# Performance work log

Measured on AMD Instinct MI355X. Metric: run time of the kernel, lower is better.

Reference implementation:

```python
import jax, jax.numpy as jnp
import numpy as np

NEG = -1.0e9  # matches torch's masked_fill value
EPS = 1e-12


def setup_inputs() -> dict:
    key = jax.random.key(0)
    ks = jax.random.split(key, 8)
    B, T, S, E, H, M = 128, 512, 512, 256, 1024, 4

    def lin_w(k, fan_in, fan_out):
        lim = 1.0 / np.sqrt(fan_in)
        return jax.random.uniform(k, (fan_in, fan_out), jnp.float32, -lim, lim)

    return {
        "state": jax.random.normal(ks[0], (B, S), jnp.float32),
        "task_features": jax.random.normal(ks[1], (B, T, 5), jnp.float32),
        "nest_ids": jax.random.randint(ks[2], (B, T), 0, M),
        "task_mask": jnp.ones((B, T), jnp.bool_),
        "emb_w": lin_w(ks[3], 5, E),
        "emb_b": jnp.zeros((E,), jnp.float32),
        "w1": lin_w(ks[4], S + E, H),
        "b1": jnp.zeros((H,), jnp.float32),
        "w2": lin_w(ks[5], H, H),
        "b2": jnp.zeros((H,), jnp.float32),
        "w3": lin_w(ks[6], H, 1),
        "b3": jnp.zeros((1,), jnp.float32),
        "etas": jnp.ones((M,), jnp.float32),  # eta_buf (learn_eta=False, eta_init=1.0)
    }


def reference(state, task_features, nest_ids, task_mask,
              emb_w, emb_b, w1, b1, w2, b2, w3, b3, etas):
    B, T, _ = task_features.shape
    M = etas.shape[0]

    # per-task utilities: MLP over concat(state, task_embed)  [B,T]
    te = task_features @ emb_w + emb_b                                # [B,T,E]
    x = jnp.concatenate(
        [jnp.broadcast_to(state[:, None, :], (B, T, state.shape[-1])), te], axis=-1)
    h = jax.nn.relu(x @ w1 + b1)
    h = jax.nn.relu(h @ w2 + b2)
    utils = (h @ w3 + b3)[..., 0]                                     # [B,T]
    utils = jnp.where(task_mask, utils, NEG)

    # nest membership masks (vectorized segment-softmax over nests)
    mem = (nest_ids[..., None] == jnp.arange(M)) & task_mask[..., None]  # [B,T,M]
    nonempty = mem.any(axis=1)                                           # [B,M]

    mval = jnp.max(jnp.where(mem, utils[..., None], -jnp.inf), axis=1)   # [B,M]
    mval = jnp.where(nonempty, mval, 0.0)
    scaled = (utils[..., None] - mval[:, None, :]) / etas                # [B,T,M]
    sums = jnp.sum(jnp.where(mem, jnp.exp(scaled), 0.0), axis=1)         # [B,M]

    # inclusive values U_m = mval + eta_m * log(sum exp((v-mval)/eta_m))
    U = jnp.where(nonempty, mval + etas * jnp.log(jnp.clip(sums, EPS)), NEG)
    p_nest = jax.nn.softmax(U, axis=-1)                                  # [B,M]

    # per-task within-nest probabilities, gathered via nest id
    nid = jnp.clip(nest_ids, 0, M - 1)
    m_t = jnp.take_along_axis(mval, nid, axis=1)                         # [B,T]
    s_t = jnp.take_along_axis(jnp.clip(sums, EPS), nid, axis=1)          # [B,T]
    pn_t = jnp.take_along_axis(p_nest, nid, axis=1)                      # [B,T]
    e_t = jnp.exp((utils - m_t) / etas[nid])
    valid = task_mask & (nest_ids >= 0) & (nest_ids < M)
    p_task = jnp.where(valid, pn_t * e_t / s_t, 0.0)                     # [B,T]

    # degenerate fallback: uniform over valid tasks when everything underflowed
    any_valid = task_mask.any(axis=1)
    fallback = any_valid & (p_task.sum(axis=1) <= EPS)
    uni = 1.0 / jnp.maximum(task_mask.sum(axis=1), 1).astype(p_task.dtype)
    p_task = jnp.where(fallback[:, None] & task_mask, uni[:, None], p_task)

    return utils, p_task, p_nest
```

## Files before the change

kernel.cpp:

```cpp
#include <hip/hip_runtime.h>
#include <stdint.h>

#define NEGV -1.0e9f
#define EPSV 1e-12f

typedef __attribute__((ext_vector_type(8))) short bf16x8;
typedef __attribute__((ext_vector_type(4))) float f32x4;

__device__ __forceinline__ unsigned int f2bf(float f) {
  unsigned int u = __builtin_bit_cast(unsigned int, f);
  u = u + 0x7FFFu + ((u >> 16) & 1u);
  return u >> 16;
}

__device__ __forceinline__ unsigned int cvt_pk_bf16(float lo, float hi) {
  unsigned int r;
  asm("v_cvt_pk_bf16_f32 %0, %1, %2" : "=v"(r) : "v"(lo), "v"(hi));
  return r;
}

__global__ __launch_bounds__(256) void k_prep(
    const float* __restrict__ state, const float* __restrict__ w1,
    const float* __restrict__ b1, const float* __restrict__ emb_w,
    const float* __restrict__ emb_b, const float* __restrict__ w2,
    float* __restrict__ W1e, float* __restrict__ sb,
    unsigned short* __restrict__ W2t) {
  const int blk = blockIdx.x;
  const int tid = threadIdx.x;
  if (blk < 4) {
    const int j = blk * 256 + tid;
    float a0 = 0.f, a1 = 0.f, a2 = 0.f, a3 = 0.f, a4 = 0.f;
    for (int e = 0; e < 256; ++e) {
      const float w = w1[(size_t)(512 + e) * 1024 + j];
      a0 += emb_w[0 * 256 + e] * w;
      a1 += emb_w[1 * 256 + e] * w;
      a2 += emb_w[2 * 256 + e] * w;
      a3 += emb_w[3 * 256 + e] * w;
      a4 += emb_w[4 * 256 + e] * w;
    }
    W1e[0 * 1024 + j] = a0;
    W1e[1 * 1024 + j] = a1;
    W1e[2 * 1024 + j] = a2;
    W1e[3 * 1024 + j] = a3;
    W1e[4 * 1024 + j] = a4;
  } else if (blk < 516) {
    const int blk2 = blk - 4;
    const int b = blk2 >> 2;
    const int j = (blk2 & 3) * 256 + tid;
    float acc = b1[j];
    for (int e = 0; e < 256; ++e)
      acc += emb_b[e] * w1[(size_t)(512 + e) * 1024 + j];
    const float* st = state + (size_t)b * 512;
    for (int s = 0; s < 512; ++s) acc += st[s] * w1[(size_t)s * 1024 + j];
    sb[(size_t)b * 1024 + j] = acc;
  } else {
    __shared__ float tile[64][65];
    const int blk2 = blk - 516;
    const int gn = blk2 & 15, gk = blk2 >> 4;
    const int c = tid & 63, w = tid >> 6;
#pragma unroll
    for (int i = 0; i < 16; ++i) {
      const int r = i * 4 + w;
      tile[r][c] = w2[(size_t)(gk * 64 + r) * 1024 + gn * 64 + c];
    }
    __syncthreads();
#pragma unroll
    for (int i = 0; i < 16; ++i) {
      const int r = i * 4 + w;
      W2t[(size_t)(gn * 64 + r) * 1024 + gk * 64 + c] = (unsigned short)f2bf(tile[c][r]);
    }
  }
}

__global__ __launch_bounds__(256) void k_h1(
    const float* __restrict__ tf, const float* __restrict__ sbm,
    const float* __restrict__ W1em, unsigned short* __restrict__ H1) {
  const int tid = threadIdx.x;
  const int j0 = (tid & 127) << 3;
  const int r0 = (blockIdx.x * 2 + (tid >> 7)) * 8;
  const int b = r0 >> 9;
  const float* sbp = sbm + (size_t)b * 1024 + j0;
  const float4 sa = *(const float4*)(sbp);
  const float4 sbv = *(const float4*)(sbp + 4);
  float4 wa[5], wb[5];
#pragma unroll
  for (int i = 0; i < 5; ++i) {
    wa[i] = *(const float4*)(W1em + i * 1024 + j0);
    wb[i] = *(const float4*)(W1em + i * 1024 + j0 + 4);
  }
#pragma unroll
  for (int r = 0; r < 8; ++r) {
    const float* f = tf + (size_t)(r0 + r) * 5;
    const float f0 = f[0], f1 = f[1], f2 = f[2], f3 = f[3], f4 = f[4];
    float h0 = fmaf(f4, wa[4].x, fmaf(f3, wa[3].x, fmaf(f2, wa[2].x, fmaf(f1, wa[1].x, fmaf(f0, wa[0].x, sa.x)))));
    float h1 = fmaf(f4, wa[4].y, fmaf(f3, wa[3].y, fmaf(f2, wa[2].y, fmaf(f1, wa[1].y, fmaf(f0, wa[0].y, sa.y)))));
    float h2 = fmaf(f4, wa[4].z, fmaf(f3, wa[3].z, fmaf(f2, wa[2].z, fmaf(f1, wa[1].z, fmaf(f0, wa[0].z, sa.z)))));
    float h3 = fmaf(f4, wa[4].w, fmaf(f3, wa[3].w, fmaf(f2, wa[2].w, fmaf(f1, wa[1].w, fmaf(f0, wa[0].w, sa.w)))));
    float h4 = fmaf(f4, wb[4].x, fmaf(f3, wb[3].x, fmaf(f2, wb[2].x, fmaf(f1, wb[1].x, fmaf(f0, wb[0].x, sbv.x)))));
    float h5 = fmaf(f4, wb[4].y, fmaf(f3, wb[3].y, fmaf(f2, wb[2].y, fmaf(f1, wb[1].y, fmaf(f0, wb[0].y, sbv.y)))));
    float h6 = fmaf(f4, wb[4].z, fmaf(f3, wb[3].z, fmaf(f2, wb[2].z, fmaf(f1, wb[1].z, fmaf(f0, wb[0].z, sbv.z)))));
    float h7 = fmaf(f4, wb[4].w, fmaf(f3, wb[3].w, fmaf(f2, wb[2].w, fmaf(f1, wb[1].w, fmaf(f0, wb[0].w, sbv.w)))));
    h0 = fmaxf(h0, 0.f); h1 = fmaxf(h1, 0.f); h2 = fmaxf(h2, 0.f); h3 = fmaxf(h3, 0.f);
    h4 = fmaxf(h4, 0.f); h5 = fmaxf(h5, 0.f); h6 = fmaxf(h6, 0.f); h7 = fmaxf(h7, 0.f);
    uint4 pk;
    pk.x = cvt_pk_bf16(h0, h1);
    pk.y = cvt_pk_bf16(h2, h3);
    pk.z = cvt_pk_bf16(h4, h5);
    pk.w = cvt_pk_bf16(h6, h7);
    *(uint4*)&H1[(size_t)(r0 + r) * 1024 + j0] = pk;
  }
}

__global__ __launch_bounds__(512, 2) void k_gemm2(
    const unsigned short* __restrict__ H1, const unsigned short* __restrict__ W2t,
    const float* __restrict__ b2, const float* __restrict__ w3,
    float* __restrict__ partial) {
  __shared__ unsigned short As[2][16384];
  __shared__ unsigned short Bs[2][16384];

  const int bid = blockIdx.x;
  const int swz = (bid & 7) * 128 + (bid >> 3);
  const int bx = swz >> 2, by = swz & 3;
  const int row0 = bx << 8, col0 = by << 8;

  const int tid = threadIdx.x, lane = tid & 63, wid = tid >> 6;

  const int sr = (wid << 5) + (lane >> 3);
  const int scol = (((lane & 7) ^ ((lane >> 3) & 7)) << 3);
  const size_t abase = (size_t)(row0 + sr) * 1024 + scol;
  const size_t bbase = (size_t)(col0 + sr) * 1024 + scol;
  const int ldsb = (wid << 5) * 64;

#define STAGE8(kt, d)                                                         \
    _Pragma("unroll")                                                         \
    for (int q = 0; q < 4; ++q) {                                             \
      __builtin_amdgcn_global_load_lds(                                       \
          (const __attribute__((address_space(1))) void*)(                    \
              H1 + abase + (size_t)q * 8192 + (kt) * 64),                     \
          (__attribute__((address_space(3))) void*)(As[d] + ldsb + q * 512),  \
          16, 0, 0);                                                          \
      __builtin_amdgcn_global_load_lds(                                       \
          (const __attribute__((address_space(1))) void*)(                    \
              W2t + bbase + (size_t)q * 8192 + (kt) * 64),                    \
          (__attribute__((address_space(3))) void*)(Bs[d] + ldsb + q * 512),  \
          16, 0, 0);                                                          \
    }

#define STAGE2(kt, d, q)                                                      \
    {                                                                         \
      __builtin_amdgcn_global_load_lds(                                       \
          (const __attribute__((address_space(1))) void*)(                    \
              H1 + abase + (size_t)(q) * 8192 + (kt) * 64),                   \
          (__attribute__((address_space(3))) void*)(As[d] + ldsb + (q) * 512),\
          16, 0, 0);                                                          \
      __builtin_amdgcn_global_load_lds(                                       \
          (const __attribute__((address_space(1))) void*)(                    \
              W2t + bbase + (size_t)(q) * 8192 + (kt) * 64),                  \
          (__attribute__((address_space(3))) void*)(Bs[d] + ldsb + (q) * 512),\
          16, 0, 0);                                                          \
    }

  const int wr = wid >> 2, wc = wid & 3;
  const int lm = lane & 15, lg = lane >> 4;
  const int aoff = (wr * 128 + lm) * 64;
  const int boff = (wc * 64 + lm) * 64;
  const int s0 = ((lg ^ (lm & 7)) << 3);
  const int s1 = (((4 + lg) ^ (lm & 7)) << 3);

  f32x4 acc[8][4];
#pragma unroll
  for (int m = 0; m < 8; ++m)
#pragma unroll
    for (int n = 0; n < 4; ++n) acc[m][n] = (f32x4){0.f, 0.f, 0.f, 0.f};

  STAGE8(0, 0);
  __syncthreads();

#pragma unroll 1
  for (int t = 0; t < 16; ++t) {
    const unsigned short* Ad = As[t & 1];
    const unsigned short* Bd = Bs[t & 1];
    bf16x8 bk0[4], bk1[4];
#pragma unroll
    for (int p = 0; p < 4; ++p) {
      if (p == 0) {
#pragma unroll
        for (int n = 0; n < 4; ++n) {
          bk0[n] = *(const bf16x8*)(Bd + boff + n * 1024 + s0);
          bk1[n] = *(const bf16x8*)(Bd + boff + n * 1024 + s1);
        }
      }
      bf16x8 a0k0 = *(const bf16x8*)(Ad + aoff + (2 * p) * 1024 + s0);
      bf16x8 a0k1 = *(const bf16x8*)(Ad + aoff + (2 * p) * 1024 + s1);
      bf16x8 a1k0 = *(const bf16x8*)(Ad + aoff + (2 * p + 1) * 1024 + s0);
      bf16x8 a1k1 = *(const bf16x8*)(Ad + aoff + (2 * p + 1) * 1024 + s1);
      if (t < 15) STAGE2(t + 1, (t + 1) & 1, p);
      __builtin_amdgcn_s_barrier();
      asm volatile("s_waitcnt lgkmcnt(0)" ::: "memory");
      __builtin_amdgcn_sched_barrier(0);
      __builtin_amdgcn_s_setprio(1);
#pragma unroll
      for (int n = 0; n < 4; ++n)
        acc[2 * p][n] = __builtin_amdgcn_mfma_f32_16x16x32_bf16(a0k0, bk0[n], acc[2 * p][n], 0, 0, 0);
#pragma unroll
      for (int n = 0; n < 4; ++n)
        acc[2 * p][n] = __builtin_amdgcn_mfma_f32_16x16x32_bf16(a0k1, bk1[n], acc[2 * p][n], 0, 0, 0);
#pragma unroll
      for (int n = 0; n < 4; ++n)
        acc[2 * p + 1][n] = __builtin_amdgcn_mfma_f32_16x16x32_bf16(a1k0, bk0[n], acc[2 * p + 1][n], 0, 0, 0);
#pragma unroll
      for (int n = 0; n < 4; ++n)
        acc[2 * p + 1][n] = __builtin_amdgcn_mfma_f32_16x16x32_bf16(a1k1, bk1[n], acc[2 * p + 1][n], 0, 0, 0);
      __builtin_amdgcn_s_setprio(0);
      if (p == 3 && t < 15) asm volatile("s_waitcnt vmcnt(0)" ::: "memory");
      __builtin_amdgcn_s_barrier();
    }
  }
#undef STAGE8
#undef STAGE2

  float b2v[4], w3v[4];
#pragma unroll
  for (int n = 0; n < 4; ++n) {
    const int col = col0 + wc * 64 + n * 16 + lm;
    b2v[n] = b2[col];
    w3v[n] = w3[col];
  }
#pragma unroll
  for (int m = 0; m < 8; ++m) {
#pragma unroll
    for (int r = 0; r < 4; ++r) {
      float v = 0.f;
#pragma unroll
      for (int n = 0; n < 4; ++n) {
        float h = acc[m][n][r] + b2v[n];
        h = fmaxf(h, 0.f);
        v += h * w3v[n];
      }
      v += __shfl_xor(v, 1, 16);
      v += __shfl_xor(v, 2, 16);
      v += __shfl_xor(v, 4, 16);
      v += __shfl_xor(v, 8, 16);
      if (lm == 0)
        partial[(size_t)(row0 + wr * 128 + m * 16 + lg * 4 + r) * 16 + by * 4 + wc] = v;
    }
  }
}

__global__ __launch_bounds__(256) void k_softmax(
    const float* __restrict__ partial, const float* __restrict__ b3,
    const int* __restrict__ nids, const int* __restrict__ mask,
    const float* __restrict__ etas, float* __restrict__ utils_out,
    float* __restrict__ p_task, float* __restrict__ p_nest) {
  const int b = blockIdx.x, tid = threadIdx.x;
  const int lane = tid & 63, wv = tid >> 6;
  __shared__ float smax[4][4];
  __shared__ int scnt[4][4];
  __shared__ float ssum[4][4];
  __shared__ float sred[4];
  __shared__ int sredi[4];

  const size_t base = (size_t)b * 512;
  const float b3v = b3[0];
  float uraw[2];
#pragma unroll
  for (int k = 0; k < 2; ++k) {
    const size_t row = base + tid + k * 256;
    const float4* p = (const float4*)(partial + row * 16);
    const float4 pa = p[0], pb = p[1], pc = p[2], pd = p[3];
    uraw[k] = b3v + pa.x + pa.y + pa.z + pa.w + pb.x + pb.y + pb.z + pb.w +
              pc.x + pc.y + pc.z + pc.w + pd.x + pd.y + pd.z + pd.w;
  }
  const int n0 = nids[base + tid], n1 = nids[base + 256 + tid];
  const bool m0 = mask[base + tid] != 0, m1 = mask[base + 256 + tid] != 0;
  const float u0 = m0 ? uraw[0] : NEGV;
  const float u1 = m1 ? uraw[1] : NEGV;
  utils_out[base + tid] = u0;
  utils_out[base + 256 + tid] = u1;
  const float eta[4] = {etas[0], etas[1], etas[2], etas[3]};

  float lmax[4]; int lcnt[4];
#pragma unroll
  for (int m = 0; m < 4; ++m) {
    const bool e0 = m0 && (n0 == m), e1 = m1 && (n1 == m);
    lmax[m] = fmaxf(e0 ? u0 : -INFINITY, e1 ? u1 : -INFINITY);
    lcnt[m] = (int)e0 + (int)e1;
  }
#pragma unroll
  for (int m = 0; m < 4; ++m)
#pragma unroll
    for (int off = 32; off >= 1; off >>= 1) {
      lmax[m] = fmaxf(lmax[m], __shfl_xor(lmax[m], off));
      lcnt[m] += __shfl_xor(lcnt[m], off);
    }
  if (lane == 0) {
#pragma unroll
    for (int m = 0; m < 4; ++m) { smax[wv][m] = lmax[m]; scnt[wv][m] = lcnt[m]; }
  }
  __syncthreads();
  float mval[4]; bool ne[4];
#pragma unroll
  for (int m = 0; m < 4; ++m) {
    const float mx = fmaxf(fmaxf(smax[0][m], smax[1][m]), fmaxf(smax[2][m], smax[3][m]));
    const int c = scnt[0][m] + scnt[1][m] + scnt[2][m] + scnt[3][m];
    ne[m] = c > 0;
    mval[m] = ne[m] ? mx : 0.f;
  }
  float lsum[4];
#pragma unroll
  for (int m = 0; m < 4; ++m) {
    float s = 0.f;
    if (m0 && n0 == m) s += expf((u0 - mval[m]) / eta[m]);
    if (m1 && n1 == m) s += expf((u1 - mval[m]) / eta[m]);
    lsum[m] = s;
  }
#pragma unroll
  for (int m = 0; m < 4; ++m)
#pragma unroll
    for (int off = 32; off >= 1; off >>= 1) lsum[m] += __shfl_xor(lsum[m], off);
  if (lane == 0) {
#pragma unroll
    for (int m = 0; m < 4; ++m) ssum[wv][m] = lsum[m];
  }
  __syncthreads();
  float sums[4], U[4];
#pragma unroll
  for (int m = 0; m < 4; ++m) {
    const float s = ssum[0][m] + ssum[1][m] + ssum[2][m] + ssum[3][m];
    sums[m] = fmaxf(s, EPSV);
    U[m] = ne[m] ? (mval[m] + eta[m] * logf(sums[m])) : NEGV;
  }
  const float mU = fmaxf(fmaxf(U[0], U[1]), fmaxf(U[2], U[3]));
  float pe[4], pes = 0.f;
#pragma unroll
  for (int m = 0; m < 4; ++m) { pe[m] = expf(U[m] - mU); pes += pe[m]; }
  float pn[4];
#pragma unroll
  for (int m = 0; m < 4; ++m) pn[m] = pe[m] / pes;
  if (tid == 0) {
#pragma unroll
    for (int m = 0; m < 4; ++m) p_nest[(size_t)b * 4 + m] = pn[m];
  }
  float pt[2];
  const float uu[2] = {u0, u1};
  const int nn[2] = {n0, n1};
  const bool mm[2] = {m0, m1};
#pragma unroll
  for (int k = 0; k < 2; ++k) {
    const bool valid = mm[k] && nn[k] >= 0 && nn[k] < 4;
    float mt = 0.f, st = 1.f, pnt = 0.f, et = 1.f;
#pragma unroll
    for (int m = 0; m < 4; ++m)
      if (nn[k] == m) { mt = mval[m]; st = sums[m]; pnt = pn[m]; et = eta[m]; }
    pt[k] = valid ? pnt * expf((uu[k] - mt) / et) / st : 0.f;
  }
  float lp = pt[0] + pt[1];
  int lmk = (int)m0 + (int)m1;
#pragma unroll
  for (int off = 32; off >= 1; off >>= 1) {
    lp += __shfl_xor(lp, off);
    lmk += __shfl_xor(lmk, off);
  }
  if (lane == 0) { sred[wv] = lp; sredi[wv] = lmk; }
  __syncthreads();
  const float sumpt = sred[0] + sred[1] + sred[2] + sred[3];
  const int nmask = sredi[0] + sredi[1] + sredi[2] + sredi[3];
  const bool fallback = (nmask > 0) && (sumpt <= EPSV);
  if (fallback) {
    const float uni = 1.f / (float)(nmask > 0 ? nmask : 1);
    pt[0] = m0 ? uni : pt[0];
    pt[1] = m1 ? uni : pt[1];
  }
  p_task[base + tid] = pt[0];
  p_task[base + 256 + tid] = pt[1];
}

extern "C" void kernel_launch(void* const* d_in, const int* in_sizes, int n_in,
                              void* d_out, int out_size, void* d_ws, size_t ws_size,
                              hipStream_t stream) {
  const float* state = (const float*)d_in[0];
  const float* tf = (const float*)d_in[1];
  const int* nids = (const int*)d_in[2];
  const int* mask = (const int*)d_in[3];
  const float* emb_w = (const float*)d_in[4];
  const float* emb_b = (const float*)d_in[5];
  const float* w1 = (const float*)d_in[6];
  const float* b1 = (const float*)d_in[7];
  const float* w2 = (const float*)d_in[8];
  const float* b2 = (const float*)d_in[9];
  const float* w3 = (const float*)d_in[10];
  const float* b3 = (const float*)d_in[11];
  const float* etas = (const float*)d_in[12];

  float* out = (float*)d_out;
  float* utils_out = out;
  float* p_task = out + 65536;
  float* p_nest = out + 131072;

  char* ws = (char*)d_ws;
  unsigned short* W2t = (unsigned short*)ws; ws += 1024ull * 1024 * 2;
  float* partial = (float*)ws;               ws += 65536ull * 16 * 4;
  float* W1e = (float*)ws;                   ws += 5 * 1024 * 4;
  float* sb = (float*)ws;                    ws += 128 * 1024 * 4;
  unsigned short* H1 = (unsigned short*)ws;  ws += 65536ull * 1024 * 2;

  k_prep<<<772, 256, 0, stream>>>(state, w1, b1, emb_w, emb_b, w2, W1e, sb, W2t);
  k_h1<<<4096, 256, 0, stream>>>(tf, sb, W1e, H1);
  k_gemm2<<<1024, 512, 0, stream>>>(H1, W2t, b2, w3, partial);
  k_softmax<<<128, 256, 0, stream>>>(partial, b3, nids, mask, etas,
                                     utils_out, p_task, p_nest);
}
```

Measured before the change: 188.3 us.

## Deepen GEMM2 LDS pipeline to four K=32 stages with partial vmcnt waits

The second-layer GEMM kernel moves from a double buffer of K=64 tiles to a four-slot ring of K=32 half-tiles in LDS, with a new swizzle and load mapping. It issues loads three half-tiles ahead and waits with vmcnt(8) instead of draining all outstanding loads, so global loads overlap MFMA work across more stages. In exchange it adds more barriers per K step and more intricate wait accounting, and LDS use stays at the same total size.

```diff
diff --git a/kernel.cpp b/kernel.cpp
--- a/kernel.cpp
+++ b/kernel.cpp
@@ -115,8 +115,8 @@
     const unsigned short* __restrict__ H1, const unsigned short* __restrict__ W2t,
     const float* __restrict__ b2, const float* __restrict__ w3,
     float* __restrict__ partial) {
-  __shared__ unsigned short As[2][16384];
-  __shared__ unsigned short Bs[2][16384];
+  __shared__ unsigned short As[4][8192];
+  __shared__ unsigned short Bs[4][8192];
 
   const int bid = blockIdx.x;
   const int swz = (bid & 7) * 128 + (bid >> 3);
@@ -125,47 +125,29 @@
 
   const int tid = threadIdx.x, lane = tid & 63, wid = tid >> 6;
 
-  const int sr = (wid << 5) + (lane >> 3);
-  const int scol = (((lane & 7) ^ ((lane >> 3) & 7)) << 3);
-  const size_t abase = (size_t)(row0 + sr) * 1024 + scol;
-  const size_t bbase = (size_t)(col0 + sr) * 1024 + scol;
-  const int ldsb = (wid << 5) * 64;
-
-#define STAGE8(kt, d)                                                         \
-    _Pragma("unroll")                                                         \
-    for (int q = 0; q < 4; ++q) {                                             \
-      __builtin_amdgcn_global_load_lds(                                       \
-          (const __attribute__((address_space(1))) void*)(                    \
-              H1 + abase + (size_t)q * 8192 + (kt) * 64),                     \
-          (__attribute__((address_space(3))) void*)(As[d] + ldsb + q * 512),  \
-          16, 0, 0);                                                          \
-      __builtin_amdgcn_global_load_lds(                                       \
-          (const __attribute__((address_space(1))) void*)(                    \
-              W2t + bbase + (size_t)q * 8192 + (kt) * 64),                    \
-          (__attribute__((address_space(3))) void*)(Bs[d] + ldsb + q * 512),  \
-          16, 0, 0);                                                          \
-    }
-
-#define STAGE2(kt, d, q)                                                      \
+  const int rwrow = (wid << 4) + (lane >> 2);
+  const int srcsw = (((lane & 3) ^ ((lane >> 3) & 3)) << 3);
+  const int ldstb = wid << 9;
+
+#define STAGEH(hh, q)                                                         \
     {                                                                         \
       __builtin_amdgcn_global_load_lds(                                       \
           (const __attribute__((address_space(1))) void*)(                    \
-              H1 + abase + (size_t)(q) * 8192 + (kt) * 64),                   \
-          (__attribute__((address_space(3))) void*)(As[d] + ldsb + (q) * 512),\
-          16, 0, 0);                                                          \
+              H1 + (size_t)(row0 + (q) * 128 + rwrow) * 1024 + (hh) * 32 + srcsw), \
+          (__attribute__((address_space(3))) void*)(                          \
+              As[(hh) & 3] + (q) * 4096 + ldstb), 16, 0, 0);                  \
       __builtin_amdgcn_global_load_lds(                                       \
           (const __attribute__((address_space(1))) void*)(                    \
-              W2t + bbase + (size_t)(q) * 8192 + (kt) * 64),                  \
-          (__attribute__((address_space(3))) void*)(Bs[d] + ldsb + (q) * 512),\
-          16, 0, 0);                                                          \
+              W2t + (size_t)(col0 + (q) * 128 + rwrow) * 1024 + (hh) * 32 + srcsw), \
+          (__attribute__((address_space(3))) void*)(                          \
+              Bs[(hh) & 3] + (q) * 4096 + ldstb), 16, 0, 0);                  \
     }
 
   const int wr = wid >> 2, wc = wid & 3;
   const int lm = lane & 15, lg = lane >> 4;
-  const int aoff = (wr * 128 + lm) * 64;
-  const int boff = (wc * 64 + lm) * 64;
-  const int s0 = ((lg ^ (lm & 7)) << 3);
-  const int s1 = (((4 + lg) ^ (lm & 7)) << 3);
+  const int aoff = (wr * 128 + lm) * 32;
+  const int boff = (wc * 64 + lm) * 32;
+  const int s = ((lg ^ ((lm >> 1) & 3)) << 3);
 
   f32x4 acc[8][4];
 #pragma unroll
@@ -173,51 +155,53 @@
 #pragma unroll
     for (int n = 0; n < 4; ++n) acc[m][n] = (f32x4){0.f, 0.f, 0.f, 0.f};
 
-  STAGE8(0, 0);
-  __syncthreads();
+  STAGEH(0, 0); STAGEH(0, 1);
+  STAGEH(1, 0); STAGEH(1, 1);
+  STAGEH(2, 0); STAGEH(2, 1);
+  asm volatile("s_waitcnt vmcnt(8)" ::: "memory");
+  __builtin_amdgcn_s_barrier();
 
 #pragma unroll 1
   for (int t = 0; t < 16; ++t) {
-    const unsigned short* Ad = As[t & 1];
-    const unsigned short* Bd = Bs[t & 1];
-    bf16x8 bk0[4], bk1[4];
-#pragma unroll
-    for (int p = 0; p < 4; ++p) {
-      if (p == 0) {
-#pragma unroll
-        for (int n = 0; n < 4; ++n) {
-          bk0[n] = *(const bf16x8*)(Bd + boff + n * 1024 + s0);
-          bk1[n] = *(const bf16x8*)(Bd + boff + n * 1024 + s1);
+#pragma unroll
+    for (int half = 0; half < 2; ++half) {
+      const unsigned short* Ad = As[(2 * t + half) & 3];
+      const unsigned short* Bd = Bs[(2 * t + half) & 3];
+      bf16x8 bk[4];
+#pragma unroll
+      for (int n = 0; n < 4; ++n) bk[n] = *(const bf16x8*)(Bd + boff + n * 512 + s);
+#pragma unroll
+      for (int ph = 0; ph < 2; ++ph) {
+        bf16x8 av[4];
+#pragma unroll
+        for (int i = 0; i < 4; ++i)
+          av[i] = *(const bf16x8*)(Ad + aoff + (ph * 4 + i) * 512 + s);
+        const int hh = 2 * t + 3 + half;
+        if (hh < 32) STAGEH(hh, ph);
+        __builtin_amdgcn_s_barrier();
+        asm volatile("s_waitcnt lgkmcnt(0)" ::: "memory");
+        __builtin_amdgcn_s_setprio(1);
+#pragma unroll
+        for (int i = 0; i < 4; ++i)
+#pragma unroll
+          for (int n = 0; n < 4; ++n)
+            acc[ph * 4 + i][n] = __builtin_amdgcn_mfma_f32_16x16x32_bf16(
+                av[i], bk[n], acc[ph * 4 + i][n], 0, 0, 0);
+        __builtin_amdgcn_s_setprio(0);
+        if (ph == 1) {
+          if (half == 0) {
+            if (t < 15) { asm volatile("s_waitcnt vmcnt(8)" ::: "memory"); }
+            else        { asm volatile("s_waitcnt vmcnt(0)" ::: "memory"); }
+          } else {
+            if (t < 14)       { asm volatile("s_waitcnt vmcnt(8)" ::: "memory"); }
+            else if (t == 14) { asm volatile("s_waitcnt vmcnt(4)" ::: "memory"); }
+          }
         }
+        __builtin_amdgcn_s_barrier();
       }
-      bf16x8 a0k0 = *(const bf16x8*)(Ad + aoff + (2 * p) * 1024 + s0);
-      bf16x8 a0k1 = *(const bf16x8*)(Ad + aoff + (2 * p) * 1024 + s1);
-      bf16x8 a1k0 = *(const bf16x8*)(Ad + aoff + (2 * p + 1) * 1024 + s0);
-      bf16x8 a1k1 = *(const bf16x8*)(Ad + aoff + (2 * p + 1) * 1024 + s1);
-      if (t < 15) STAGE2(t + 1, (t + 1) & 1, p);
-      __builtin_amdgcn_s_barrier();
-      asm volatile("s_waitcnt lgkmcnt(0)" ::: "memory");
-      __builtin_amdgcn_sched_barrier(0);
-      __builtin_amdgcn_s_setprio(1);
-#pragma unroll
-      for (int n = 0; n < 4; ++n)
-        acc[2 * p][n] = __builtin_amdgcn_mfma_f32_16x16x32_bf16(a0k0, bk0[n], acc[2 * p][n], 0, 0, 0);
-#pragma unroll
-      for (int n = 0; n < 4; ++n)
-        acc[2 * p][n] = __builtin_amdgcn_mfma_f32_16x16x32_bf16(a0k1, bk1[n], acc[2 * p][n], 0, 0, 0);
-#pragma unroll
-      for (int n = 0; n < 4; ++n)
-        acc[2 * p + 1][n] = __builtin_amdgcn_mfma_f32_16x16x32_bf16(a1k0, bk0[n], acc[2 * p + 1][n], 0, 0, 0);
-#pragma unroll
-      for (int n = 0; n < 4; ++n)
-        acc[2 * p + 1][n] = __builtin_amdgcn_mfma_f32_16x16x32_bf16(a1k1, bk1[n], acc[2 * p + 1][n], 0, 0, 0);
-      __builtin_amdgcn_s_setprio(0);
-      if (p == 3 && t < 15) asm volatile("s_waitcnt vmcnt(0)" ::: "memory");
-      __builtin_amdgcn_s_barrier();
-    }
-  }
-#undef STAGE8
-#undef STAGE2
+    }
+  }
+#undef STAGEH
 
   float b2v[4], w3v[4];
 #pragma unroll
```

Measured after the change: 192.3 us. +2.1%, slower.
